# Optimization experiments

Measured on AMD Instinct MI355X. Metric: run time of the kernel, lower is better.

The kernel has to match this reference:

```python
import jax, jax.numpy as jnp
import numpy as np

B, NV, NRINGS, NDIRS, C, F = 2, 20000, 8, 8, 16, 16


def setup_inputs() -> dict:
    key = jax.random.key(0)
    ks = jax.random.split(key, 7)
    y = jax.random.normal(ks[0], (B, NV, NDIRS, C), jnp.float32)
    contributors = jax.random.randint(ks[1], (NV, NRINGS, NDIRS, 3), 0, NV, dtype=jnp.int32)
    weights_bary = jax.random.uniform(ks[2], (NV, NRINGS, NDIRS, 3), jnp.float32)
    angles = jax.random.randint(ks[3], (NV, NRINGS, NDIRS, 3), 0, NDIRS, dtype=jnp.int32)
    kernel = jax.random.normal(ks[4], (NRINGS, NDIRS, C, F), jnp.float32) * 0.05
    center_kernel = jax.random.normal(ks[5], (C, F), jnp.float32) * 0.05
    bias = jnp.zeros((F,), jnp.float32)
    return {"y": y, "contributors": contributors, "weights_bary": weights_bary,
            "angles": angles, "kernel": kernel, "center_kernel": center_kernel, "bias": bias}


def reference(y, contributors, weights_bary, angles, kernel, center_kernel, bias):
    # y: (B, nv, ndirs, C); tables: (nv, nrings, ndirs, 3)
    b, nv, ndirs, nch = y.shape
    nfilters = kernel.shape[-1]
    nrings = contributors.shape[1]

    # window_interpolation_sync: gather 3 contributor vertices per window bin,
    # with the direction axis re-indexed per-contributor (radial sync), then
    # barycentric-weighted sum.  Flatten (vertex, dir) into one gather index.
    idx = contributors * ndirs + angles                 # (nv, nrings, ndirs, 3)
    y_flat = y.reshape(b, nv * ndirs, nch)
    gathered = y_flat[:, idx, :]                        # (B, nv, nrings, ndirs, 3, C)
    z = jnp.einsum('bvrdjc,vrdj->bvrdc', gathered, weights_bary)  # (B, nv, nrings, ndirs, C)

    # gcnn_conv: circular pad over dirs then VALID conv with (nrings, ndirs) kernel
    zr = z.reshape(b * nv, nrings, ndirs, nch)
    zr = jnp.concatenate([zr, zr[:, :, :-1, :]], axis=2)  # width 2*ndirs-1
    conv = jax.lax.conv_general_dilated(
        zr, kernel, window_strides=(1, 1), padding='VALID',
        dimension_numbers=('NHWC', 'HWIO', 'NHWC'))       # (B*nv, 1, ndirs, F)
    conv = conv.reshape(b, nv, ndirs, nfilters)

    out = conv + jnp.einsum('bvdc,cf->bvdf', y, center_kernel) + bias
    out = jax.nn.relu(out)
    return jnp.max(out, axis=2)                          # take_max over directions -> (B, nv, F)
```

## Files before the change

kernel.cpp:

```cpp
#include <hip/hip_runtime.h>

typedef unsigned short u16;
typedef __attribute__((ext_vector_type(4))) unsigned int u32x4;
typedef __attribute__((ext_vector_type(4))) float f32x4;
typedef __attribute__((ext_vector_type(8))) __bf16 bf16x8;

constexpr int BATCH = 2;
constexpr int NV    = 20000;
constexpr int NR    = 8;
constexpr int ND    = 8;
constexpr int CH    = 16;
constexpr int NF    = 16;
constexpr int NVD   = NV * ND;
constexpr int K0    = NR * ND * CH;
constexpr int KE    = K0 + ND * CH;
constexpr int NCHUNK = KE / 32;
constexpr int NN    = ND * NF;
constexpr int MV    = 64;
constexpr int ZSTR  = KE + 8;
constexpr int BSTR  = 40;
constexpr int NT_PER_B = (NV + MV - 1) / MV;

constexpr size_t Y16_ELEMS = (size_t)BATCH * NVD * CH;
constexpr size_t K2C_OFF_B = Y16_ELEMS * 2;

__device__ __forceinline__ u16 f2bf(float x) {
    unsigned int u = __float_as_uint(x);
    unsigned int r = (u + 0x7fffu + ((u >> 16) & 1u)) >> 16;
    return (u16)r;
}
__device__ __forceinline__ unsigned int pack2bf(float a, float b) {
    return (unsigned int)f2bf(a) | ((unsigned int)f2bf(b) << 16);
}

__global__ __launch_bounds__(256) void y_to_bf16(const float* __restrict__ y, u16* __restrict__ y16) {
    int i = blockIdx.x * 256 + threadIdx.x;
    const float4 v = ((const float4*)y)[i];
    unsigned int lo = pack2bf(v.x, v.y);
    unsigned int hi = pack2bf(v.z, v.w);
    ((uint2*)y16)[i] = make_uint2(lo, hi);
}

__global__ __launch_bounds__(256) void k2_build(const float* __restrict__ kern,
                                                const float* __restrict__ ck,
                                                u16* __restrict__ k2c) {
    int e = blockIdx.x * 256 + threadIdx.x;
    int i = e & 4095;
    int kc = e >> 12;
    int n = i >> 5, kk = i & 31;
    int k = kc * 32 + kk;
    int w = n >> 4, f = n & 15;
    float val;
    if (k < K0) {
        int r = k >> 7, dd = (k >> 4) & 7, c = k & 15;
        int d = (dd - w) & 7;
        val = kern[((r * 8 + d) * 16 + c) * 16 + f];
    } else {
        int ke = k - K0;
        int d = ke >> 4, c = ke & 15;
        val = (d == w) ? ck[c * 16 + f] : 0.f;
    }
    k2c[e] = f2bf(val);
}

__global__ __launch_bounds__(256, 1) void geo_main(const u16* __restrict__ y16,
                                                   const u16* __restrict__ k2c,
                                                   const int* __restrict__ contrib,
                                                   const float* __restrict__ wbary,
                                                   const int* __restrict__ angles,
                                                   const float* __restrict__ bias,
                                                   float* __restrict__ out) {
    __shared__ __align__(16) unsigned char smem[(size_t)MV * ZSTR * 2 + (size_t)NN * BSTR * 2];
    u16* zb = (u16*)smem;
    u16* Bb = (u16*)(smem + (size_t)MV * ZSTR * 2);
    int* emax = (int*)(smem + (size_t)MV * ZSTR * 2);

    const int t = threadIdx.x;
    const int bx = blockIdx.x;
    const int b = (bx >= NT_PER_B) ? 1 : 0;
    const int vt = bx - b * NT_PER_B;
    const int v0 = vt * MV;
    const int nvt = (NV - v0 < MV) ? (NV - v0) : MV;

    for (int e = t; e < MV * 16; e += 256) {
        int vl = e >> 4, i = e & 15;
        int d = i >> 1, c8 = (i & 1) * 8;
        u32x4 val = {0u, 0u, 0u, 0u};
        if (vl < nvt) {
            const u32x4* src = (const u32x4*)(y16 + ((size_t)(b * NVD + (v0 + vl) * ND + d) * CH + c8));
            val = *src;
        }
        *(u32x4*)(zb + (size_t)vl * ZSTR + K0 + d * CH + c8) = val;
    }

    for (int it = 0; it < (MV * 64) / 256; ++it) {
        int item = t + it * 256;
        int vl = item >> 6, rd = item & 63;
        float acc[CH];
        #pragma unroll
        for (int c = 0; c < CH; ++c) acc[c] = 0.f;
        if (vl < nvt) {
            size_t mbase = ((size_t)(v0 + vl) * 64 + rd) * 3;
            #pragma unroll
            for (int j = 0; j < 3; ++j) {
                int cn = contrib[mbase + j];
                int an = angles[mbase + j];
                float wj = wbary[mbase + j];
                const u16* src = y16 + ((size_t)b * NVD + cn * ND + an) * CH;
                u32x4 p0 = *(const u32x4*)(src);
                u32x4 p1 = *(const u32x4*)(src + 8);
                #pragma unroll
                for (int q = 0; q < 4; ++q) {
                    unsigned int u = p0[q];
                    acc[2 * q]     += wj * __uint_as_float(u << 16);
                    acc[2 * q + 1] += wj * __uint_as_float(u & 0xffff0000u);
                }
                #pragma unroll
                for (int q = 0; q < 4; ++q) {
                    unsigned int u = p1[q];
                    acc[8 + 2 * q]     += wj * __uint_as_float(u << 16);
                    acc[8 + 2 * q + 1] += wj * __uint_as_float(u & 0xffff0000u);
                }
            }
        }
        u32x4 o0, o1;
        #pragma unroll
        for (int q = 0; q < 4; ++q) {
            o0[q] = pack2bf(acc[2 * q], acc[2 * q + 1]);
            o1[q] = pack2bf(acc[8 + 2 * q], acc[8 + 2 * q + 1]);
        }
        u16* dst = zb + (size_t)vl * ZSTR + rd * CH;
        *(u32x4*)(dst) = o0;
        *(u32x4*)(dst + 8) = o1;
    }
    __syncthreads();

    const int wid = t >> 6, lane = t & 63;
    const int wr = wid >> 1, wc = wid & 1;
    const int lrow = lane & 15, lq = lane >> 4;

    f32x4 acc[2][4];
    #pragma unroll
    for (int rt = 0; rt < 2; ++rt)
        #pragma unroll
        for (int nt = 0; nt < 4; ++nt)
            acc[rt][nt] = (f32x4){0.f, 0.f, 0.f, 0.f};

    for (int kc = 0; kc < NCHUNK; ++kc) {
        #pragma unroll
        for (int s = 0; s < 2; ++s) {
            int e = t + s * 256;
            int n = e >> 2, q = e & 3;
            u32x4 val = *(const u32x4*)(k2c + (size_t)kc * 4096 + n * 32 + q * 8);
            *(u32x4*)(Bb + n * BSTR + q * 8) = val;
        }
        __syncthreads();

        bf16x8 af[2], bfr[4];
        #pragma unroll
        for (int rt = 0; rt < 2; ++rt) {
            int row = wr * 32 + rt * 16 + lrow;
            af[rt] = *(const bf16x8*)(zb + (size_t)row * ZSTR + kc * 32 + lq * 8);
        }
        #pragma unroll
        for (int nt = 0; nt < 4; ++nt) {
            int col = wc * 64 + nt * 16 + lrow;
            bfr[nt] = *(const bf16x8*)(Bb + col * BSTR + lq * 8);
        }
        #pragma unroll
        for (int rt = 0; rt < 2; ++rt)
            #pragma unroll
            for (int nt = 0; nt < 4; ++nt)
                acc[rt][nt] = __builtin_amdgcn_mfma_f32_16x16x32_bf16(af[rt], bfr[nt], acc[rt][nt], 0, 0, 0);
        __syncthreads();
    }

    for (int e = t; e < MV * NF; e += 256) emax[e] = 0;
    __syncthreads();
    const float bf_ = bias[lrow];
    #pragma unroll
    for (int rt = 0; rt < 2; ++rt) {
        #pragma unroll
        for (int reg = 0; reg < 4; ++reg) {
            float m = 0.f;
            #pragma unroll
            for (int nt = 0; nt < 4; ++nt) m = fmaxf(m, acc[rt][nt][reg] + bf_);
            int row = wr * 32 + rt * 16 + lq * 4 + reg;
            atomicMax(&emax[row * NF + lrow], __float_as_int(m));
        }
    }
    __syncthreads();
    for (int e = t; e < MV * NF; e += 256) {
        int vl = e >> 4, f = e & 15;
        if (vl < nvt) out[((size_t)(b * NV + v0 + vl)) * NF + f] = __int_as_float(emax[e]);
    }
}

extern "C" void kernel_launch(void* const* d_in, const int* in_sizes, int n_in,
                              void* d_out, int out_size, void* d_ws, size_t ws_size,
                              hipStream_t stream) {
    const float* y      = (const float*)d_in[0];
    const int*   contrib= (const int*)d_in[1];
    const float* wbary  = (const float*)d_in[2];
    const int*   angles = (const int*)d_in[3];
    const float* kern   = (const float*)d_in[4];
    const float* ck     = (const float*)d_in[5];
    const float* bias   = (const float*)d_in[6];
    float* out = (float*)d_out;

    u16* y16 = (u16*)d_ws;
    u16* k2c = (u16*)((char*)d_ws + K2C_OFF_B);

    y_to_bf16<<<(int)(Y16_ELEMS / 4 / 256), 256, 0, stream>>>(y, y16);
    k2_build<<<(NCHUNK * 4096) / 256, 256, 0, stream>>>(kern, ck, k2c);
    geo_main<<<BATCH * NT_PER_B, 256, 0, stream>>>(y16, k2c, contrib, wbary, angles, bias, out);
}
```

Measured before the change: 241.1 us.

## Split fused gather+GEMM kernel into separate gather and streaming GEMM kernels

Measured after the change: 216.8 us. 1.11x faster.

```diff
diff --git a/kernel.cpp b/kernel.cpp
--- a/kernel.cpp
+++ b/kernel.cpp
@@ -7,22 +7,19 @@
 
 constexpr int BATCH = 2;
 constexpr int NV    = 20000;
-constexpr int NR    = 8;
 constexpr int ND    = 8;
 constexpr int CH    = 16;
 constexpr int NF    = 16;
 constexpr int NVD   = NV * ND;
-constexpr int K0    = NR * ND * CH;
-constexpr int KE    = K0 + ND * CH;
+constexpr int K0    = 1024;
+constexpr int KE    = 1152;
 constexpr int NCHUNK = KE / 32;
-constexpr int NN    = ND * NF;
-constexpr int MV    = 64;
-constexpr int ZSTR  = KE + 8;
+constexpr int MTOT  = BATCH * NV;
 constexpr int BSTR  = 40;
-constexpr int NT_PER_B = (NV + MV - 1) / MV;
 
-constexpr size_t Y16_ELEMS = (size_t)BATCH * NVD * CH;
-constexpr size_t K2C_OFF_B = Y16_ELEMS * 2;
+constexpr size_t Y16_OFF_B = 0;
+constexpr size_t K2C_OFF_B = 10240000;
+constexpr size_t ZC_OFF_B  = 10534912;
 
 __device__ __forceinline__ u16 f2bf(float x) {
     unsigned int u = __float_as_uint(x);
@@ -33,12 +30,21 @@
     return (unsigned int)f2bf(a) | ((unsigned int)f2bf(b) << 16);
 }
 
-__global__ __launch_bounds__(256) void y_to_bf16(const float* __restrict__ y, u16* __restrict__ y16) {
-    int i = blockIdx.x * 256 + threadIdx.x;
-    const float4 v = ((const float4*)y)[i];
-    unsigned int lo = pack2bf(v.x, v.y);
-    unsigned int hi = pack2bf(v.z, v.w);
-    ((uint2*)y16)[i] = make_uint2(lo, hi);
+__global__ __launch_bounds__(256) void prep(const float* __restrict__ y,
+                                            u16* __restrict__ y16,
+                                            u16* __restrict__ zc) {
+    int tid = blockIdx.x * 256 + threadIdx.x;
+    const float4* src = (const float4*)(y + (size_t)tid * 16);
+    float4 v0 = src[0], v1 = src[1], v2 = src[2], v3 = src[3];
+    u32x4 lo = {pack2bf(v0.x, v0.y), pack2bf(v0.z, v0.w), pack2bf(v1.x, v1.y), pack2bf(v1.z, v1.w)};
+    u32x4 hi = {pack2bf(v2.x, v2.y), pack2bf(v2.z, v2.w), pack2bf(v3.x, v3.y), pack2bf(v3.z, v3.w)};
+    u16* yd = y16 + (size_t)tid * 16;
+    *(u32x4*)(yd)     = lo;
+    *(u32x4*)(yd + 8) = hi;
+    int iv = tid >> 3, d = tid & 7;
+    u16* zd = zc + ((size_t)(32 + (d >> 1)) * MTOT + iv) * 32 + (d & 1) * 16;
+    *(u32x4*)(zd)     = lo;
+    *(u32x4*)(zd + 8) = hi;
 }
 
 __global__ __launch_bounds__(256) void k2_build(const float* __restrict__ kern,
@@ -63,136 +69,109 @@
     k2c[e] = f2bf(val);
 }
 
-__global__ __launch_bounds__(256, 1) void geo_main(const u16* __restrict__ y16,
-                                                   const u16* __restrict__ k2c,
-                                                   const int* __restrict__ contrib,
-                                                   const float* __restrict__ wbary,
-                                                   const int* __restrict__ angles,
-                                                   const float* __restrict__ bias,
-                                                   float* __restrict__ out) {
-    __shared__ __align__(16) unsigned char smem[(size_t)MV * ZSTR * 2 + (size_t)NN * BSTR * 2];
-    u16* zb = (u16*)smem;
-    u16* Bb = (u16*)(smem + (size_t)MV * ZSTR * 2);
-    int* emax = (int*)(smem + (size_t)MV * ZSTR * 2);
+__global__ __launch_bounds__(256) void gather(const u16* __restrict__ y16,
+                                              const int* __restrict__ contrib,
+                                              const float* __restrict__ wbary,
+                                              const int* __restrict__ angles,
+                                              u16* __restrict__ zc) {
+    int item = blockIdx.x * 256 + threadIdx.x;
+    int iv = item >> 6, rd = item & 63;
+    int b = iv >= NV;
+    int v = iv - b * NV;
+    size_t mb = ((size_t)v * 64 + rd) * 3;
+    const u16* ybase = y16 + (size_t)b * NVD * CH;
 
+    float acc[CH];
+    #pragma unroll
+    for (int c = 0; c < CH; ++c) acc[c] = 0.f;
+    #pragma unroll
+    for (int j = 0; j < 3; ++j) {
+        int cn = contrib[mb + j];
+        int an = angles[mb + j];
+        float wj = wbary[mb + j];
+        const u16* src = ybase + ((size_t)cn * ND + an) * CH;
+        u32x4 p0 = *(const u32x4*)(src);
+        u32x4 p1 = *(const u32x4*)(src + 8);
+        #pragma unroll
+        for (int q = 0; q < 4; ++q) {
+            unsigned int u = p0[q];
+            acc[2 * q]     += wj * __uint_as_float(u << 16);
+            acc[2 * q + 1] += wj * __uint_as_float(u & 0xffff0000u);
+        }
+        #pragma unroll
+        for (int q = 0; q < 4; ++q) {
+            unsigned int u = p1[q];
+            acc[8 + 2 * q]     += wj * __uint_as_float(u << 16);
+            acc[8 + 2 * q + 1] += wj * __uint_as_float(u & 0xffff0000u);
+        }
+    }
+    u32x4 o0, o1;
+    #pragma unroll
+    for (int q = 0; q < 4; ++q) {
+        o0[q] = pack2bf(acc[2 * q], acc[2 * q + 1]);
+        o1[q] = pack2bf(acc[8 + 2 * q], acc[8 + 2 * q + 1]);
+    }
+    u16* dst = zc + ((size_t)(rd >> 1) * MTOT + iv) * 32 + (rd & 1) * 16;
+    *(u32x4*)(dst)     = o0;
+    *(u32x4*)(dst + 8) = o1;
+}
+
+__global__ __launch_bounds__(256) void gemm_max(const u16* __restrict__ zc,
+                                                const u16* __restrict__ k2c,
+                                                const float* __restrict__ bias,
+                                                float* __restrict__ out) {
+    __shared__ __align__(16) u16 Bb[2][128 * BSTR];
     const int t = threadIdx.x;
-    const int bx = blockIdx.x;
-    const int b = (bx >= NT_PER_B) ? 1 : 0;
-    const int vt = bx - b * NT_PER_B;
-    const int v0 = vt * MV;
-    const int nvt = (NV - v0 < MV) ? (NV - v0) : MV;
+    const int w = t >> 6, lane = t & 63;
+    const int lrow = lane & 15, lq = lane >> 4;
+    const int m0 = blockIdx.x * 64;
+    const int arow = m0 + w * 16 + lrow;
 
-    for (int e = t; e < MV * 16; e += 256) {
-        int vl = e >> 4, i = e & 15;
-        int d = i >> 1, c8 = (i & 1) * 8;
-        u32x4 val = {0u, 0u, 0u, 0u};
-        if (vl < nvt) {
-            const u32x4* src = (const u32x4*)(y16 + ((size_t)(b * NVD + (v0 + vl) * ND + d) * CH + c8));
-            val = *src;
+    const int sn = t >> 1, sh = (t & 1) * 16;
+
+    {
+        const u32x4* src = (const u32x4*)(k2c + (size_t)0 * 4096 + sn * 32 + sh);
+        u32x4 b0 = src[0], b1 = src[1];
+        u16* dst = &Bb[0][sn * BSTR + sh];
+        *(u32x4*)(dst)     = b0;
+        *(u32x4*)(dst + 8) = b1;
+    }
+    bf16x8 a_next = *(const bf16x8*)(zc + ((size_t)0 * MTOT + arow) * 32 + lq * 8);
+
+    f32x4 acc[8];
+    #pragma unroll
+    for (int nt = 0; nt < 8; ++nt) acc[nt] = (f32x4){0.f, 0.f, 0.f, 0.f};
+
+    for (int kc = 0; kc < NCHUNK; ++kc) {
+        __syncthreads();
+        bf16x8 a = a_next;
+        u32x4 bn0, bn1;
+        if (kc < NCHUNK - 1) {
+            a_next = *(const bf16x8*)(zc + ((size_t)(kc + 1) * MTOT + arow) * 32 + lq * 8);
+            const u32x4* src = (const u32x4*)(k2c + (size_t)(kc + 1) * 4096 + sn * 32 + sh);
+            bn0 = src[0]; bn1 = src[1];
         }
-        *(u32x4*)(zb + (size_t)vl * ZSTR + K0 + d * CH + c8) = val;
+        bf16x8 bf[8];
+        #pragma unroll
+        for (int nt = 0; nt < 8; ++nt)
+            bf[nt] = *(const bf16x8*)(&Bb[kc & 1][(nt * 16 + lrow) * BSTR + lq * 8]);
+        #pragma unroll
+        for (int nt = 0; nt < 8; ++nt)
+            acc[nt] = __builtin_amdgcn_mfma_f32_16x16x32_bf16(a, bf[nt], acc[nt], 0, 0, 0);
+        if (kc < NCHUNK - 1) {
+            u16* dst = &Bb[(kc + 1) & 1][sn * BSTR + sh];
+            *(u32x4*)(dst)     = bn0;
+            *(u32x4*)(dst + 8) = bn1;
+        }
     }
 
-    for (int it = 0; it < (MV * 64) / 256; ++it) {
-        int item = t + it * 256;
-        int vl = item >> 6, rd = item & 63;
-        float acc[CH];
+    const float bb = bias[lrow];
+    #pragma unroll
+    for (int reg = 0; reg < 4; ++reg) {
+        float m = 0.f;
         #pragma unroll
-        for (int c = 0; c < CH; ++c) acc[c] = 0.f;
-        if (vl < nvt) {
-            size_t mbase = ((size_t)(v0 + vl) * 64 + rd) * 3;
-            #pragma unroll
-            for (int j = 0; j < 3; ++j) {
-                int cn = contrib[mbase + j];
-                int an = angles[mbase + j];
-                float wj = wbary[mbase + j];
-                const u16* src = y16 + ((size_t)b * NVD + cn * ND + an) * CH;
-                u32x4 p0 = *(const u32x4*)(src);
-                u32x4 p1 = *(const u32x4*)(src + 8);
-                #pragma unroll
-                for (int q = 0; q < 4; ++q) {
-                    unsigned int u = p0[q];
-                    acc[2 * q]     += wj * __uint_as_float(u << 16);
-                    acc[2 * q + 1] += wj * __uint_as_float(u & 0xffff0000u);
-                }
-                #pragma unroll
-                for (int q = 0; q < 4; ++q) {
-                    unsigned int u = p1[q];
-                    acc[8 + 2 * q]     += wj * __uint_as_float(u << 16);
-                    acc[8 + 2 * q + 1] += wj * __uint_as_float(u & 0xffff0000u);
-                }
-            }
-        }
-        u32x4 o0, o1;
-        #pragma unroll
-        for (int q = 0; q < 4; ++q) {
-            o0[q] = pack2bf(acc[2 * q], acc[2 * q + 1]);
-            o1[q] = pack2bf(acc[8 + 2 * q], acc[8 + 2 * q + 1]);
-        }
-        u16* dst = zb + (size_t)vl * ZSTR + rd * CH;
-        *(u32x4*)(dst) = o0;
-        *(u32x4*)(dst + 8) = o1;
-    }
-    __syncthreads();
-
-    const int wid = t >> 6, lane = t & 63;
-    const int wr = wid >> 1, wc = wid & 1;
-    const int lrow = lane & 15, lq = lane >> 4;
-
-    f32x4 acc[2][4];
-    #pragma unroll
-    for (int rt = 0; rt < 2; ++rt)
-        #pragma unroll
-        for (int nt = 0; nt < 4; ++nt)
-            acc[rt][nt] = (f32x4){0.f, 0.f, 0.f, 0.f};
-
-    for (int kc = 0; kc < NCHUNK; ++kc) {
-        #pragma unroll
-        for (int s = 0; s < 2; ++s) {
-            int e = t + s * 256;
-            int n = e >> 2, q = e & 3;
-            u32x4 val = *(const u32x4*)(k2c + (size_t)kc * 4096 + n * 32 + q * 8);
-            *(u32x4*)(Bb + n * BSTR + q * 8) = val;
-        }
-        __syncthreads();
-
-        bf16x8 af[2], bfr[4];
-        #pragma unroll
-        for (int rt = 0; rt < 2; ++rt) {
-            int row = wr * 32 + rt * 16 + lrow;
-            af[rt] = *(const bf16x8*)(zb + (size_t)row * ZSTR + kc * 32 + lq * 8);
-        }
-        #pragma unroll
-        for (int nt = 0; nt < 4; ++nt) {
-            int col = wc * 64 + nt * 16 + lrow;
-            bfr[nt] = *(const bf16x8*)(Bb + col * BSTR + lq * 8);
-        }
-        #pragma unroll
-        for (int rt = 0; rt < 2; ++rt)
-            #pragma unroll
-            for (int nt = 0; nt < 4; ++nt)
-                acc[rt][nt] = __builtin_amdgcn_mfma_f32_16x16x32_bf16(af[rt], bfr[nt], acc[rt][nt], 0, 0, 0);
-        __syncthreads();
-    }
-
-    for (int e = t; e < MV * NF; e += 256) emax[e] = 0;
-    __syncthreads();
-    const float bf_ = bias[lrow];
-    #pragma unroll
-    for (int rt = 0; rt < 2; ++rt) {
-        #pragma unroll
-        for (int reg = 0; reg < 4; ++reg) {
-            float m = 0.f;
-            #pragma unroll
-            for (int nt = 0; nt < 4; ++nt) m = fmaxf(m, acc[rt][nt][reg] + bf_);
-            int row = wr * 32 + rt * 16 + lq * 4 + reg;
-            atomicMax(&emax[row * NF + lrow], __float_as_int(m));
-        }
-    }
-    __syncthreads();
-    for (int e = t; e < MV * NF; e += 256) {
-        int vl = e >> 4, f = e & 15;
-        if (vl < nvt) out[((size_t)(b * NV + v0 + vl)) * NF + f] = __int_as_float(emax[e]);
+        for (int nt = 0; nt < 8; ++nt) m = fmaxf(m, acc[nt][reg] + bb);
+        out[((size_t)(m0 + w * 16 + lq * 4 + reg)) * NF + lrow] = m;
     }
 }
 
@@ -208,10 +187,12 @@
     const float* bias   = (const float*)d_in[6];
     float* out = (float*)d_out;
 
-    u16* y16 = (u16*)d_ws;
+    u16* y16 = (u16*)((char*)d_ws + Y16_OFF_B);
     u16* k2c = (u16*)((char*)d_ws + K2C_OFF_B);
+    u16* zc  = (u16*)((char*)d_ws + ZC_OFF_B);
 
-    y_to_bf16<<<(int)(Y16_ELEMS / 4 / 256), 256, 0, stream>>>(y, y16);
+    prep<<<1250, 256, 0, stream>>>(y, y16, zc);
     k2_build<<<(NCHUNK * 4096) / 256, 256, 0, stream>>>(kern, ck, k2c);
-    geo_main<<<BATCH * NT_PER_B, 256, 0, stream>>>(y16, k2c, contrib, wbary, angles, bias, out);
+    gather<<<10000, 256, 0, stream>>>(y16, contrib, wbary, angles, zc);
+    gemm_max<<<MTOT / 64, 256, 0, stream>>>(zc, k2c, bias, out);
 }
```
